# Kernel optimization log

Hardware: AMD Instinct MI355X
Metric: run time of the kernel (lower is better)

The kernel has to match this reference:

```python
import jax, jax.numpy as jnp
import numpy as np

NEG_SLOPE = 0.2


def gat_conv(x, src, dst, W, att_src, att_dst, bias, heads, out_ch, concat):
    """PyG-style GATConv (eval mode, self-loops already appended to src/dst)."""
    N = x.shape[0]
    h = (x @ W).reshape(N, heads, out_ch)                      # [N,H,C]
    a_src = jnp.einsum('nhc,hc->nh', h, att_src)               # [N,H]
    a_dst = jnp.einsum('nhc,hc->nh', h, att_dst)               # [N,H]
    e = jax.nn.leaky_relu(a_src[src] + a_dst[dst], NEG_SLOPE)  # [E,H]
    # numerically-stable softmax segmented by destination node
    emax = jax.ops.segment_max(e, dst, num_segments=N)         # [N,H]
    e = jnp.exp(e - emax[dst])
    denom = jax.ops.segment_sum(e, dst, num_segments=N)
    alpha = e / (denom[dst] + 1e-16)                           # [E,H]
    msg = h[src] * alpha[..., None]                            # [E,H,C]
    out = jax.ops.segment_sum(msg, dst, num_segments=N)        # [N,H,C]
    out = out.reshape(N, heads * out_ch) if concat else out.mean(axis=1)
    return out + bias


def setup_inputs() -> dict:
    key = jax.random.key(0)
    ks = jax.random.split(key, 9)
    N, E, IN, OUT = 100000, 1600000, 128, 40
    H1, C1 = 8, 8
    x = jax.random.normal(ks[0], (N, IN), dtype=jnp.float32)
    edge_index = jax.random.randint(ks[1], (2, E), 0, N, dtype=jnp.int64)
    s = 0.1
    return {
        'x': x,
        'edge_index': edge_index,
        'W1': jax.random.normal(ks[2], (IN, H1 * C1), dtype=jnp.float32) * s,
        'att_src1': jax.random.normal(ks[3], (H1, C1), dtype=jnp.float32) * s,
        'att_dst1': jax.random.normal(ks[4], (H1, C1), dtype=jnp.float32) * s,
        'b1': jnp.zeros((H1 * C1,), dtype=jnp.float32),
        'W2': jax.random.normal(ks[5], (H1 * C1, OUT), dtype=jnp.float32) * s,
        'att_src2': jax.random.normal(ks[6], (1, OUT), dtype=jnp.float32) * s,
        'att_dst2': jax.random.normal(ks[7], (1, OUT), dtype=jnp.float32) * s,
        'b2': jnp.zeros((OUT,), dtype=jnp.float32),
    }


def reference(x, edge_index, W1, att_src1, att_dst1, b1, W2, att_src2, att_dst2, b2):
    N = x.shape[0]
    loops = jnp.arange(N, dtype=edge_index.dtype)
    src = jnp.concatenate([edge_index[0], loops])  # self-loops (PyG default)
    dst = jnp.concatenate([edge_index[1], loops])
    h = gat_conv(x, src, dst, W1, att_src1, att_dst1, b1, 8, 8, True)
    h = jax.nn.elu(h)  # dropout is identity in eval mode
    out = gat_conv(h, src, dst, W2, att_src2, att_dst2, b2, 1, W2.shape[1], False)
    return jax.nn.log_softmax(out, axis=-1)
```

## Files before the change

### kernel.cpp

```cpp
#include <hip/hip_runtime.h>
#include <math.h>

#define NEG_SLOPE 0.2f
#define BSHIFT 8
#define MAXBUK 512

typedef __attribute__((ext_vector_type(8))) short short8;
typedef __attribute__((ext_vector_type(4))) float floatx4;

static __device__ __forceinline__ float lrelu_exp(float e) {
    e = fmaxf(e, NEG_SLOPE * e);
    return __expf(e);
}

static __device__ __forceinline__ short f2bf(float f) {
    union { float f; unsigned u; } v; v.f = f;
    unsigned r = v.u + 0x7FFFu + ((v.u >> 16) & 1u);
    return (short)(r >> 16);
}
static __device__ __forceinline__ float bf2f(unsigned short s) {
    union { float f; unsigned u; } v;
    v.u = ((unsigned)s) << 16;
    return v.f;
}
static __device__ __forceinline__ float bfpair_lo(unsigned v) {
    union { float f; unsigned u; } x; x.u = v << 16; return x.f;
}
static __device__ __forceinline__ float bfpair_hi(unsigned v) {
    union { float f; unsigned u; } x; x.u = v & 0xffff0000u; return x.f;
}
static __device__ __forceinline__ void splitbf(float f, short& hi, short& lo) {
    hi = f2bf(f);
    lo = f2bf(f - bf2f((unsigned short)hi));
}


__global__ __launch_bounds__(512) void k_hist(const int* __restrict__ dst, int E, int CHUNK,
                                              int NBLK, int NBUK, int* __restrict__ blockhist) {
    __shared__ int hist[MAXBUK];
    int t = threadIdx.x, b = blockIdx.x;
    for (int i = t; i < NBUK; i += 512) hist[i] = 0;
    __syncthreads();
    int e0 = b * CHUNK, e1 = e0 + CHUNK; if (e1 > E) e1 = E;
    for (int e = e0 + t; e < e1; e += 512) atomicAdd(&hist[dst[e] >> BSHIFT], 1);
    __syncthreads();
    for (int i = t; i < NBUK; i += 512) blockhist[(size_t)i * NBLK + b] = hist[i];
}

__global__ __launch_bounds__(256) void k_colscan(int* __restrict__ blockhist,
                                                 int* __restrict__ btot, int NBLK) {
    int bucket = blockIdx.x, t = threadIdx.x;
    int lane = t & 63, wv = t >> 6;
    __shared__ int wsum[4];
    __shared__ int carry_s;
    if (t == 0) carry_s = 0;
    __syncthreads();
    for (int base = 0; base < NBLK; base += 256) {
        int idx = base + t;
        int v = (idx < NBLK) ? blockhist[(size_t)bucket * NBLK + idx] : 0;
        int s = v;
#pragma unroll
        for (int o = 1; o < 64; o <<= 1) {
            int u = __shfl_up(s, o, 64);
            if (lane >= o) s += u;
        }
        if (lane == 63) wsum[wv] = s;
        __syncthreads();
        int b0 = 0;
#pragma unroll
        for (int w = 0; w < 4; ++w) b0 += (w < wv) ? wsum[w] : 0;
        int excl = s + b0 - v + carry_s;
        if (idx < NBLK) blockhist[(size_t)bucket * NBLK + idx] = excl;
        __syncthreads();
        if (t == 255) carry_s += s + b0;
        __syncthreads();
    }
    if (t == 0) btot[bucket] = carry_s;
}

__global__ __launch_bounds__(512) void k_bucket_scan(const int* __restrict__ btot,
                                                     int* __restrict__ bucketbase, int NBUK) {
    __shared__ int sh[512];
    int t = threadIdx.x;
    int v = (t < NBUK) ? btot[t] : 0;
    sh[t] = v;
    __syncthreads();
#pragma unroll
    for (int o = 1; o < 512; o <<= 1) {
        int u = (t >= o) ? sh[t - o] : 0;
        __syncthreads();
        sh[t] += u;
        __syncthreads();
    }
    if (t < NBUK) bucketbase[t] = sh[t] - v;
    if (t == NBUK - 1) bucketbase[NBUK] = sh[t];
}

__global__ __launch_bounds__(512) void k_partition(const int* __restrict__ src,
                                                   const int* __restrict__ dst, int E, int CHUNK,
                                                   int NBLK, int NBUK,
                                                   const int* __restrict__ blockhist,
                                                   const int* __restrict__ bucketbase,
                                                   unsigned* __restrict__ packed) {
    __shared__ int cur[MAXBUK];
    int t = threadIdx.x, b = blockIdx.x;
    for (int i = t; i < NBUK; i += 512)
        cur[i] = blockhist[(size_t)i * NBLK + b] + bucketbase[i];
    __syncthreads();
    int e0 = b * CHUNK, e1 = e0 + CHUNK; if (e1 > E) e1 = E;
    for (int e = e0 + t; e < e1; e += 512) {
        int d = dst[e], s = src[e];
        int pos = atomicAdd(&cur[d >> BSHIFT], 1);
        packed[pos] = ((unsigned)s << 8) | ((unsigned)d & 255u);
    }
}

__global__ __launch_bounds__(256) void k_fine(const unsigned* __restrict__ packed,
                                              const int* __restrict__ bucketbase,
                                              int* __restrict__ offsets,
                                              int* __restrict__ csr_src,
                                              int N, int NBUK) {
    __shared__ int fcnt[256];
    __shared__ int wsum[4];
    int bucket = blockIdx.x, t = threadIdx.x;
    int lo = bucket << BSHIFT;
    int nn = N - lo; if (nn > 256) nn = 256;
    int ebase = bucketbase[bucket];
    int ecnt = bucketbase[bucket + 1] - ebase;
    fcnt[t] = 0;
    __syncthreads();
    for (int i = t; i < ecnt; i += 256) {
        unsigned p = packed[ebase + i];
        atomicAdd(&fcnt[p & 255u], 1);
    }
    __syncthreads();
    int v = fcnt[t];
    int lane = t & 63, wv = t >> 6;
    int s = v;
#pragma unroll
    for (int o = 1; o < 64; o <<= 1) {
        int u = __shfl_up(s, o, 64);
        if (lane >= o) s += u;
    }
    if (lane == 63) wsum[wv] = s;
    __syncthreads();
    int base = 0;
#pragma unroll
    for (int w = 0; w < 4; ++w) base += (w < wv) ? wsum[w] : 0;
    int excl = s + base - v;
    if (t < nn) offsets[lo + t] = ebase + excl;
    if (bucket == NBUK - 1 && t == 0) offsets[N] = ebase + ecnt;
    __syncthreads();
    fcnt[t] = excl;
    __syncthreads();
    for (int i = t; i < ecnt; i += 256) {
        unsigned p = packed[ebase + i];
        int pos = atomicAdd(&fcnt[p & 255u], 1);
        csr_src[ebase + pos] = (int)(p >> 8);
    }
}

__global__ __launch_bounds__(256) void k_prepW1(const float* __restrict__ W1,
                                                short* __restrict__ w1t) {
    int i = blockIdx.x * 256 + threadIdx.x;
    if (i < 64 * 128) {
        int n = i >> 7, k = i & 127;
        w1t[i] = f2bf(W1[k * 64 + n]);
    }
}

__global__ __launch_bounds__(256) void k_splitW2(const float* __restrict__ W2,
                                                 short* __restrict__ w2ht,
                                                 short* __restrict__ w2lt) {
    int i = blockIdx.x * 256 + threadIdx.x;
    if (i < 48 * 64) {
        int n = i >> 6, k = i & 63;
        short hi = 0, lo = 0;
        if (n < 40) splitbf(W2[k * 40 + n], hi, lo);
        w2ht[i] = hi; w2lt[i] = lo;
    }
}

__global__ __launch_bounds__(256) void k_gemm1(const float* __restrict__ x,
                                               const short* __restrict__ w1t,
                                               const float* __restrict__ att_s,
                                               const float* __restrict__ att_d,
                                               unsigned short* __restrict__ h1b,
                                               float* __restrict__ a_s1,
                                               float* __restrict__ a_d1, int N) {
    int tid = threadIdx.x, wave = tid >> 6, lane = tid & 63;
    int n16 = lane & 15, q = lane >> 4;
    int nb = blockIdx.x * 64 + wave * 16;
    if (nb >= N) return;

    short8 bfr[4][4];
#pragma unroll
    for (int ct = 0; ct < 4; ++ct) {
        int n = ct * 16 + n16;
#pragma unroll
        for (int kc = 0; kc < 4; ++kc)
            bfr[ct][kc] = *(const short8*)(w1t + n * 128 + kc * 32 + q * 8);
    }

    int arow = nb + n16; if (arow >= N) arow = N - 1;
    const float* xr = x + (size_t)arow * 128 + q * 8;
    short8 afr[4];
#pragma unroll
    for (int kc = 0; kc < 4; ++kc) {
        float4 u0 = *(const float4*)(xr + kc * 32);
        float4 u1 = *(const float4*)(xr + kc * 32 + 4);
        short8 a;
        a[0] = f2bf(u0.x); a[1] = f2bf(u0.y); a[2] = f2bf(u0.z); a[3] = f2bf(u0.w);
        a[4] = f2bf(u1.x); a[5] = f2bf(u1.y); a[6] = f2bf(u1.z); a[7] = f2bf(u1.w);
        afr[kc] = a;
    }

    floatx4 acc[4];
#pragma unroll
    for (int ct = 0; ct < 4; ++ct) {
        floatx4 c = {0.f, 0.f, 0.f, 0.f};
#pragma unroll
        for (int kc = 0; kc < 4; ++kc)
            c = __builtin_amdgcn_mfma_f32_16x16x32_bf16(afr[kc], bfr[ct][kc], c, 0, 0, 0);
        acc[ct] = c;
    }

#pragma unroll
    for (int ct = 0; ct < 4; ++ct) {
#pragma unroll
        for (int r = 0; r < 4; ++r) {
            int row = nb + q * 4 + r;
            if (row < N) h1b[(size_t)row * 64 + ct * 16 + n16] = (unsigned short)f2bf(acc[ct][r]);
        }
    }

#pragma unroll
    for (int ct = 0; ct < 4; ++ct) {
        float as = att_s[ct * 16 + n16];
        float ad = att_d[ct * 16 + n16];
#pragma unroll
        for (int r = 0; r < 4; ++r) {
            float ps = acc[ct][r] * as;
            float pd = acc[ct][r] * ad;
#pragma unroll
            for (int m = 1; m < 8; m <<= 1) {
                ps += __shfl_xor(ps, m, 64);
                pd += __shfl_xor(pd, m, 64);
            }
            int row = nb + q * 4 + r;
            if ((n16 & 7) == 0 && row < N) {
                int h = 2 * ct + (n16 >> 3);
                a_s1[row * 8 + h] = ps;
                a_d1[row * 8 + h] = pd;
            }
        }
    }
}

__global__ __launch_bounds__(256) void k_agg1(const unsigned short* __restrict__ h1b,
                                              const float* __restrict__ a_s1,
                                              const float* __restrict__ a_d1,
                                              const int* __restrict__ offsets,
                                              const int* __restrict__ csr_src,
                                              const float* __restrict__ b1,
                                              float* __restrict__ y1, int N) {
    int wave = threadIdx.x >> 6, lane = threadIdx.x & 63;
    int q = lane >> 4;
    int ll = lane & 15;
    int d = (blockIdx.x * 4 + wave) * 4 + q;
    bool dvalid = (d < N);
    int de = dvalid ? d : N - 1;
    int g = ll >> 3;
    int c = ll & 7;
    float ad = a_d1[de * 8 + c];
    int i0 = offsets[de];
    int deg = dvalid ? (offsets[de + 1] - i0) : 0;
    int dmax = deg;
    dmax = max(dmax, __shfl_xor(dmax, 16, 64));
    dmax = max(dmax, __shfl_xor(dmax, 32, 64));
    float acc[8] = {0.f, 0.f, 0.f, 0.f, 0.f, 0.f, 0.f, 0.f};
    float wsum_l = 0.f;
    if (g == 0) {
        float w0 = lrelu_exp(a_s1[de * 8 + c] + ad);
        uint4 v = *(const uint4*)(h1b + (size_t)de * 64 + 8 * c);
        acc[0] = w0 * bfpair_lo(v.x); acc[1] = w0 * bfpair_hi(v.x);
        acc[2] = w0 * bfpair_lo(v.y); acc[3] = w0 * bfpair_hi(v.y);
        acc[4] = w0 * bfpair_lo(v.z); acc[5] = w0 * bfpair_hi(v.z);
        acc[6] = w0 * bfpair_lo(v.w); acc[7] = w0 * bfpair_hi(v.w);
        wsum_l = w0;
    }
    for (int j = 0; j < dmax; j += 8) {
        int b0 = i0 + j + 4 * g;
        int idx[4]; bool lv[4];
#pragma unroll
        for (int u = 0; u < 4; ++u) {
            int jj = j + 4 * g + u;
            lv[u] = (jj < deg);
            idx[u] = de;
            if (lv[u]) idx[u] = csr_src[b0 + u];
        }
        float ev[4];
#pragma unroll
        for (int u = 0; u < 4; ++u) ev[u] = a_s1[idx[u] * 8 + c] + ad;
        uint4 vv[4];
#pragma unroll
        for (int u = 0; u < 4; ++u)
            vv[u] = *(const uint4*)(h1b + (size_t)idx[u] * 64 + 8 * c);
#pragma unroll
        for (int u = 0; u < 4; ++u) {
            float w = lv[u] ? lrelu_exp(ev[u]) : 0.f;
            wsum_l += w;
            acc[0] = fmaf(w, bfpair_lo(vv[u].x), acc[0]);
            acc[1] = fmaf(w, bfpair_hi(vv[u].x), acc[1]);
            acc[2] = fmaf(w, bfpair_lo(vv[u].y), acc[2]);
            acc[3] = fmaf(w, bfpair_hi(vv[u].y), acc[3]);
            acc[4] = fmaf(w, bfpair_lo(vv[u].z), acc[4]);
            acc[5] = fmaf(w, bfpair_hi(vv[u].z), acc[5]);
            acc[6] = fmaf(w, bfpair_lo(vv[u].w), acc[6]);
            acc[7] = fmaf(w, bfpair_hi(vv[u].w), acc[7]);
        }
    }
#pragma unroll
    for (int k = 0; k < 8; ++k) acc[k] += __shfl(acc[k], lane + 8, 64);
    wsum_l += __shfl(wsum_l, lane + 8, 64);
    if (g == 0 && dvalid) {
        float inv = 1.f / (wsum_l + 1e-16f);
        float4 bA = *(const float4*)(b1 + 8 * c);
        float4 bB = *(const float4*)(b1 + 8 * c + 4);
        float o[8];
        o[0] = acc[0] * inv + bA.x;
        o[1] = acc[1] * inv + bA.y;
        o[2] = acc[2] * inv + bA.z;
        o[3] = acc[3] * inv + bA.w;
        o[4] = acc[4] * inv + bB.x;
        o[5] = acc[5] * inv + bB.y;
        o[6] = acc[6] * inv + bB.z;
        o[7] = acc[7] * inv + bB.w;
#pragma unroll
        for (int k = 0; k < 8; ++k) o[k] = o[k] > 0.f ? o[k] : (__expf(o[k]) - 1.f);
        float4 s0 = make_float4(o[0], o[1], o[2], o[3]);
        float4 s1 = make_float4(o[4], o[5], o[6], o[7]);
        *(float4*)(y1 + (size_t)d * 64 + 8 * c) = s0;
        *(float4*)(y1 + (size_t)d * 64 + 8 * c + 4) = s1;
    }
}

__global__ __launch_bounds__(256) void k_gemm2(const float* __restrict__ y1,
                                               const short* __restrict__ w2ht,
                                               const short* __restrict__ w2lt,
                                               const float* __restrict__ att_s,
                                               const float* __restrict__ att_d,
                                               unsigned short* __restrict__ h2b,
                                               float* __restrict__ a2s,
                                               float* __restrict__ a2d, int N) {
    int tid = threadIdx.x, wave = tid >> 6, lane = tid & 63;
    int n16 = lane & 15, q = lane >> 4;
    int nb = blockIdx.x * 64 + wave * 16;
    if (nb >= N) return;

    int arow = nb + n16; if (arow >= N) arow = N - 1;
    const float* yr = y1 + (size_t)arow * 64 + q * 8;
    short8 ah[2], al[2];
#pragma unroll
    for (int kc = 0; kc < 2; ++kc) {
        float4 u0 = *(const float4*)(yr + kc * 32);
        float4 u1 = *(const float4*)(yr + kc * 32 + 4);
        short8 h, l; short hi, lo;
        splitbf(u0.x, hi, lo); h[0] = hi; l[0] = lo;
        splitbf(u0.y, hi, lo); h[1] = hi; l[1] = lo;
        splitbf(u0.z, hi, lo); h[2] = hi; l[2] = lo;
        splitbf(u0.w, hi, lo); h[3] = hi; l[3] = lo;
        splitbf(u1.x, hi, lo); h[4] = hi; l[4] = lo;
        splitbf(u1.y, hi, lo); h[5] = hi; l[5] = lo;
        splitbf(u1.z, hi, lo); h[6] = hi; l[6] = lo;
        splitbf(u1.w, hi, lo); h[7] = hi; l[7] = lo;
        ah[kc] = h; al[kc] = l;
    }

    float psr[4] = {0.f, 0.f, 0.f, 0.f}, pdr[4] = {0.f, 0.f, 0.f, 0.f};
#pragma unroll
    for (int ct = 0; ct < 3; ++ct) {
        int n = ct * 16 + n16;
        short8 bh0 = *(const short8*)(w2ht + n * 64 + q * 8);
        short8 bh1 = *(const short8*)(w2ht + n * 64 + 32 + q * 8);
        short8 bl0 = *(const short8*)(w2lt + n * 64 + q * 8);
        short8 bl1 = *(const short8*)(w2lt + n * 64 + 32 + q * 8);
        floatx4 c = {0.f, 0.f, 0.f, 0.f};
        c = __builtin_amdgcn_mfma_f32_16x16x32_bf16(ah[0], bl0, c, 0, 0, 0);
        c = __builtin_amdgcn_mfma_f32_16x16x32_bf16(al[0], bh0, c, 0, 0, 0);
        c = __builtin_amdgcn_mfma_f32_16x16x32_bf16(ah[0], bh0, c, 0, 0, 0);
        c = __builtin_amdgcn_mfma_f32_16x16x32_bf16(ah[1], bl1, c, 0, 0, 0);
        c = __builtin_amdgcn_mfma_f32_16x16x32_bf16(al[1], bh1, c, 0, 0, 0);
        c = __builtin_amdgcn_mfma_f32_16x16x32_bf16(ah[1], bh1, c, 0, 0, 0);

        int col = ct * 16 + n16;
#pragma unroll
        for (int r = 0; r < 4; ++r) {
            int row = nb + q * 4 + r;
            if (col < 40 && row < N) h2b[(size_t)row * 40 + col] = (unsigned short)f2bf(c[r]);
        }
        float asv = (col < 40) ? att_s[col] : 0.f;
        float adv = (col < 40) ? att_d[col] : 0.f;
#pragma unroll
        for (int r = 0; r < 4; ++r) {
            psr[r] = fmaf(c[r], asv, psr[r]);
            pdr[r] = fmaf(c[r], adv, pdr[r]);
        }
    }
#pragma unroll
    for (int r = 0; r < 4; ++r) {
        float ps = psr[r], pd = pdr[r];
#pragma unroll
        for (int m = 1; m < 16; m <<= 1) {
            ps += __shfl_xor(ps, m, 64);
            pd += __shfl_xor(pd, m, 64);
        }
        int row = nb + q * 4 + r;
        if (n16 == 0 && row < N) { a2s[row] = ps; a2d[row] = pd; }
    }
}

__global__ __launch_bounds__(256) void k_agg2(const unsigned short* __restrict__ h2b,
                                              const float* __restrict__ a2s,
                                              const float* __restrict__ a2d,
                                              const int* __restrict__ offsets,
                                              const int* __restrict__ csr_src,
                                              const float* __restrict__ b2,
                                              float* __restrict__ out, int N) {
    int wave = threadIdx.x >> 6, lane = threadIdx.x & 63;
    int q = lane >> 4;
    int ll = lane & 15;
    int d = (blockIdx.x * 4 + wave) * 4 + q;
    bool dvalid = (d < N);
    int de = dvalid ? d : N - 1;
    int g = ll / 5;
    int c = ll - g * 5;
    bool lane_ok = (ll < 15);
    float ad = a2d[de];
    float w0 = lrelu_exp(a2s[de] + ad);
    int i0 = offsets[de];
    int deg = offsets[de + 1] - i0;
    if (!dvalid) deg = 0;
    int dmax = deg;
    dmax = max(dmax, __shfl_xor(dmax, 16, 64));
    dmax = max(dmax, __shfl_xor(dmax, 32, 64));
    float acc[8] = {0.f, 0.f, 0.f, 0.f, 0.f, 0.f, 0.f, 0.f};
    float wsum_l = 0.f;
    if (g == 0) {
        uint4 v = *(const uint4*)(h2b + (size_t)de * 40 + 8 * c);
        acc[0] = w0 * bfpair_lo(v.x); acc[1] = w0 * bfpair_hi(v.x);
        acc[2] = w0 * bfpair_lo(v.y); acc[3] = w0 * bfpair_hi(v.y);
        acc[4] = w0 * bfpair_lo(v.z); acc[5] = w0 * bfpair_hi(v.z);
        acc[6] = w0 * bfpair_lo(v.w); acc[7] = w0 * bfpair_hi(v.w);
    }
    for (int j = 0; j < dmax; j += 12) {
        int b0 = i0 + j + 4 * g;
        int idx[4]; bool lv[4];
#pragma unroll
        for (int u = 0; u < 4; ++u) {
            int jj = j + 4 * g + u;
            lv[u] = lane_ok && (jj < deg);
            idx[u] = de;
            if (lv[u]) idx[u] = csr_src[b0 + u];
        }
        float ev[4];
#pragma unroll
        for (int u = 0; u < 4; ++u) ev[u] = a2s[idx[u]] + ad;
        uint4 vv[4];
#pragma unroll
        for (int u = 0; u < 4; ++u)
            vv[u] = *(const uint4*)(h2b + (size_t)idx[u] * 40 + 8 * c);
#pragma unroll
        for (int u = 0; u < 4; ++u) {
            float w = lv[u] ? lrelu_exp(ev[u]) : 0.f;
            if (c == 0) wsum_l += w;
            acc[0] = fmaf(w, bfpair_lo(vv[u].x), acc[0]);
            acc[1] = fmaf(w, bfpair_hi(vv[u].x), acc[1]);
            acc[2] = fmaf(w, bfpair_lo(vv[u].y), acc[2]);
            acc[3] = fmaf(w, bfpair_hi(vv[u].y), acc[3]);
            acc[4] = fmaf(w, bfpair_lo(vv[u].z), acc[4]);
            acc[5] = fmaf(w, bfpair_hi(vv[u].z), acc[5]);
            acc[6] = fmaf(w, bfpair_lo(vv[u].w), acc[6]);
            acc[7] = fmaf(w, bfpair_hi(vv[u].w), acc[7]);
        }
    }
#pragma unroll
    for (int k = 0; k < 8; ++k)
        acc[k] += __shfl(acc[k], lane + 5, 64) + __shfl(acc[k], lane + 10, 64);
    wsum_l += __shfl(wsum_l, lane + 5, 64) + __shfl(wsum_l, lane + 10, 64);
    wsum_l = __shfl(wsum_l, lane & 48, 64);
    float wsum = wsum_l + w0;
    bool act5 = (ll < 5) && dvalid;
    float inv = 1.f / (wsum + 1e-16f);
    float4 bA = *(const float4*)(b2 + 8 * c);
    float4 bB = *(const float4*)(b2 + 8 * c + 4);
    float o[8];
    o[0] = acc[0] * inv + bA.x;
    o[1] = acc[1] * inv + bA.y;
    o[2] = acc[2] * inv + bA.z;
    o[3] = acc[3] * inv + bA.w;
    o[4] = acc[4] * inv + bB.x;
    o[5] = acc[5] * inv + bB.y;
    o[6] = acc[6] * inv + bB.z;
    o[7] = acc[7] * inv + bB.w;
    float mxl = -INFINITY;
    if (act5) {
        mxl = fmaxf(fmaxf(fmaxf(o[0], o[1]), fmaxf(o[2], o[3])),
                    fmaxf(fmaxf(o[4], o[5]), fmaxf(o[6], o[7])));
    }
#pragma unroll
    for (int mm = 1; mm < 8; mm <<= 1) mxl = fmaxf(mxl, __shfl_xor(mxl, mm, 64));
    float exl = 0.f;
    if (act5) {
#pragma unroll
        for (int k = 0; k < 8; ++k) exl += __expf(o[k] - mxl);
    }
#pragma unroll
    for (int mm = 1; mm < 8; mm <<= 1) exl += __shfl_xor(exl, mm, 64);
    if (act5) {
        float lse = mxl + __logf(exl);
        float4 s0 = make_float4(o[0] - lse, o[1] - lse, o[2] - lse, o[3] - lse);
        float4 s1 = make_float4(o[4] - lse, o[5] - lse, o[6] - lse, o[7] - lse);
        *(float4*)(out + (size_t)d * 40 + 8 * c) = s0;
        *(float4*)(out + (size_t)d * 40 + 8 * c + 4) = s1;
    }
}


extern "C" void kernel_launch(void* const* d_in, const int* in_sizes, int n_in,
                              void* d_out, int out_size, void* d_ws, size_t ws_size,
                              hipStream_t stream) {
    const float* x   = (const float*)d_in[0];
    const int*   ei  = (const int*)d_in[1];
    const float* W1  = (const float*)d_in[2];
    const float* as1 = (const float*)d_in[3];
    const float* ad1 = (const float*)d_in[4];
    const float* b1  = (const float*)d_in[5];
    const float* W2  = (const float*)d_in[6];
    const float* as2 = (const float*)d_in[7];
    const float* ad2 = (const float*)d_in[8];
    const float* b2  = (const float*)d_in[9];
    float* out = (float*)d_out;

    int N = in_sizes[0] / 128;
    int E = in_sizes[1] / 2;
    const int* src = ei;
    const int* dst = ei + E;

    int NBUK = (N + 255) >> BSHIFT;
    int CHUNK = 4096;
    int NBLK = (E + CHUNK - 1) / CHUNK;

    char* ws = (char*)d_ws;
    size_t off = 0;
    auto alloc = [&](size_t bytes) -> char* {
        char* p = ws + off;
        off += (bytes + 255) & ~(size_t)255;
        return p;
    };
    unsigned short* h1b = (unsigned short*)alloc((size_t)N * 64 * 2);
    float* a_s1    = (float*)alloc((size_t)N * 8 * 4);
    float* a_d1    = (float*)alloc((size_t)N * 8 * 4);
    float* y1      = (float*)alloc((size_t)N * 64 * 4);
    size_t shared_sz = (size_t)N * 40 * 2;
    if ((size_t)E * 4 > shared_sz) shared_sz = (size_t)E * 4;
    char*  region  = alloc(shared_sz);
    unsigned short* h2b = (unsigned short*)region;
    unsigned* packed    = (unsigned*)region;
    float* a2s     = (float*)alloc((size_t)N * 4);
    float* a2d     = (float*)alloc((size_t)N * 4);
    int*   offsets = (int*)alloc((size_t)(N + 1) * 4);
    int*   csr_src = (int*)alloc((size_t)E * 4);
    int*   blockhist  = (int*)alloc((size_t)NBUK * NBLK * 4);
    int*   btot       = (int*)alloc((size_t)NBUK * 4);
    int*   bucketbase = (int*)alloc((size_t)(NBUK + 1) * 4);
    short* w1t     = (short*)alloc((size_t)64 * 128 * 2);
    short* w2ht    = (short*)alloc((size_t)48 * 64 * 2);
    short* w2lt    = (short*)alloc((size_t)48 * 64 * 2);

    int nb1 = (N + 15) / 16;
    int nb2 = (N + 15) / 16;
    int gb = (N + 63) / 64;

    k_hist<<<NBLK, 512, 0, stream>>>(dst, E, CHUNK, NBLK, NBUK, blockhist);
    k_colscan<<<NBUK, 256, 0, stream>>>(blockhist, btot, NBLK);
    k_bucket_scan<<<1, 512, 0, stream>>>(btot, bucketbase, NBUK);
    k_partition<<<NBLK, 512, 0, stream>>>(src, dst, E, CHUNK, NBLK, NBUK, blockhist,
                                          bucketbase, packed);
    k_fine<<<NBUK, 256, 0, stream>>>(packed, bucketbase, offsets, csr_src, N, NBUK);
    k_prepW1<<<32, 256, 0, stream>>>(W1, w1t);
    k_splitW2<<<12, 256, 0, stream>>>(W2, w2ht, w2lt);
    k_gemm1<<<gb, 256, 0, stream>>>(x, w1t, as1, ad1, h1b, a_s1, a_d1, N);
    k_agg1<<<nb1, 256, 0, stream>>>(h1b, a_s1, a_d1, offsets, csr_src, b1, y1, N);
    k_gemm2<<<gb, 256, 0, stream>>>(y1, w2ht, w2lt, as2, ad2, h2b, a2s, a2d, N);
    k_agg2<<<nb2, 256, 0, stream>>>(h2b, a2s, a2d, offsets, csr_src, b2, out, N);
}
```

Baseline: 180.0 us.

## Fuse weight prep into histogram and gemm1 into partition launches

Weight conversion blocks are appended to the histogram kernel, and the first-layer GEMM blocks are appended to the partition kernel, so the two independent streams of work share launches and overlap. This removes three kernel launches and lets the dense GEMM fill the GPU while the scatter-heavy partition runs. The h2b row stride is also padded from 40 to 48 elements for aligned gathers, at the cost of extra memory and bandwidth. The gemm1 part now uses 512-thread blocks covering 128 rows.

```diff
diff --git a/kernel.cpp b/kernel.cpp
--- a/kernel.cpp
+++ b/kernel.cpp
@@ -35,16 +35,36 @@
 }
 
 
-__global__ __launch_bounds__(512) void k_hist(const int* __restrict__ dst, int E, int CHUNK,
-                                              int NBLK, int NBUK, int* __restrict__ blockhist) {
+__global__ __launch_bounds__(512) void k_hist_prep(const int* __restrict__ dst, int E, int CHUNK,
+                                                   int NBLK, int NBUK,
+                                                   int* __restrict__ blockhist,
+                                                   const float* __restrict__ W1,
+                                                   short* __restrict__ w1t,
+                                                   const float* __restrict__ W2,
+                                                   short* __restrict__ w2ht,
+                                                   short* __restrict__ w2lt) {
     __shared__ int hist[MAXBUK];
     int t = threadIdx.x, b = blockIdx.x;
-    for (int i = t; i < NBUK; i += 512) hist[i] = 0;
-    __syncthreads();
-    int e0 = b * CHUNK, e1 = e0 + CHUNK; if (e1 > E) e1 = E;
-    for (int e = e0 + t; e < e1; e += 512) atomicAdd(&hist[dst[e] >> BSHIFT], 1);
-    __syncthreads();
-    for (int i = t; i < NBUK; i += 512) blockhist[(size_t)i * NBLK + b] = hist[i];
+    if (b < NBLK) {
+        for (int i = t; i < NBUK; i += 512) hist[i] = 0;
+        __syncthreads();
+        int e0 = b * CHUNK, e1 = e0 + CHUNK; if (e1 > E) e1 = E;
+        for (int e = e0 + t; e < e1; e += 512) atomicAdd(&hist[dst[e] >> BSHIFT], 1);
+        __syncthreads();
+        for (int i = t; i < NBUK; i += 512) blockhist[(size_t)i * NBLK + b] = hist[i];
+    } else {
+        int i = (b - NBLK) * 512 + t;
+        if (i < 64 * 128) {
+            int n = i >> 7, k = i & 127;
+            w1t[i] = f2bf(W1[k * 64 + n]);
+        } else if (i < 64 * 128 + 48 * 64) {
+            int j = i - 64 * 128;
+            int n = j >> 6, k = j & 63;
+            short hi = 0, lo = 0;
+            if (n < 40) splitbf(W2[k * 40 + n], hi, lo);
+            w2ht[j] = hi; w2lt[j] = lo;
+        }
+    }
 }
 
 __global__ __launch_bounds__(256) void k_colscan(int* __restrict__ blockhist,
@@ -96,22 +116,99 @@
     if (t == NBUK - 1) bucketbase[NBUK] = sh[t];
 }
 
-__global__ __launch_bounds__(512) void k_partition(const int* __restrict__ src,
-                                                   const int* __restrict__ dst, int E, int CHUNK,
-                                                   int NBLK, int NBUK,
-                                                   const int* __restrict__ blockhist,
-                                                   const int* __restrict__ bucketbase,
-                                                   unsigned* __restrict__ packed) {
+__global__ __launch_bounds__(512) void k_part_gemm1(const int* __restrict__ src,
+                                                    const int* __restrict__ dst, int E, int CHUNK,
+                                                    int NBLK, int NBUK,
+                                                    const int* __restrict__ blockhist,
+                                                    const int* __restrict__ bucketbase,
+                                                    unsigned* __restrict__ packed,
+                                                    const float* __restrict__ x,
+                                                    const short* __restrict__ w1t,
+                                                    const float* __restrict__ att_s,
+                                                    const float* __restrict__ att_d,
+                                                    unsigned short* __restrict__ h1b,
+                                                    float* __restrict__ a_s1,
+                                                    float* __restrict__ a_d1, int N) {
     __shared__ int cur[MAXBUK];
     int t = threadIdx.x, b = blockIdx.x;
-    for (int i = t; i < NBUK; i += 512)
-        cur[i] = blockhist[(size_t)i * NBLK + b] + bucketbase[i];
-    __syncthreads();
-    int e0 = b * CHUNK, e1 = e0 + CHUNK; if (e1 > E) e1 = E;
-    for (int e = e0 + t; e < e1; e += 512) {
-        int d = dst[e], s = src[e];
-        int pos = atomicAdd(&cur[d >> BSHIFT], 1);
-        packed[pos] = ((unsigned)s << 8) | ((unsigned)d & 255u);
+    if (b < NBLK) {
+        for (int i = t; i < NBUK; i += 512)
+            cur[i] = blockhist[(size_t)i * NBLK + b] + bucketbase[i];
+        __syncthreads();
+        int e0 = b * CHUNK, e1 = e0 + CHUNK; if (e1 > E) e1 = E;
+        for (int e = e0 + t; e < e1; e += 512) {
+            int d = dst[e], s = src[e];
+            int pos = atomicAdd(&cur[d >> BSHIFT], 1);
+            packed[pos] = ((unsigned)s << 8) | ((unsigned)d & 255u);
+        }
+        return;
+    }
+    int wave = t >> 6, lane = t & 63;
+    int n16 = lane & 15, q = lane >> 4;
+    int nb = (b - NBLK) * 128 + wave * 16;
+    if (nb >= N) return;
+
+    short8 bfr[4][4];
+#pragma unroll
+    for (int ct = 0; ct < 4; ++ct) {
+        int n = ct * 16 + n16;
+#pragma unroll
+        for (int kc = 0; kc < 4; ++kc)
+            bfr[ct][kc] = *(const short8*)(w1t + n * 128 + kc * 32 + q * 8);
+    }
+
+    int arow = nb + n16; if (arow >= N) arow = N - 1;
+    const float* xr = x + (size_t)arow * 128 + q * 8;
+    short8 afr[4];
+#pragma unroll
+    for (int kc = 0; kc < 4; ++kc) {
+        float4 u0 = *(const float4*)(xr + kc * 32);
+        float4 u1 = *(const float4*)(xr + kc * 32 + 4);
+        short8 a;
+        a[0] = f2bf(u0.x); a[1] = f2bf(u0.y); a[2] = f2bf(u0.z); a[3] = f2bf(u0.w);
+        a[4] = f2bf(u1.x); a[5] = f2bf(u1.y); a[6] = f2bf(u1.z); a[7] = f2bf(u1.w);
+        afr[kc] = a;
+    }
+
+    floatx4 acc[4];
+#pragma unroll
+    for (int ct = 0; ct < 4; ++ct) {
+        floatx4 c = {0.f, 0.f, 0.f, 0.f};
+#pragma unroll
+        for (int kc = 0; kc < 4; ++kc)
+            c = __builtin_amdgcn_mfma_f32_16x16x32_bf16(afr[kc], bfr[ct][kc], c, 0, 0, 0);
+        acc[ct] = c;
+    }
+
+#pragma unroll
+    for (int ct = 0; ct < 4; ++ct) {
+#pragma unroll
+        for (int r = 0; r < 4; ++r) {
+            int row = nb + q * 4 + r;
+            if (row < N) h1b[(size_t)row * 64 + ct * 16 + n16] = (unsigned short)f2bf(acc[ct][r]);
+        }
+    }
+
+#pragma unroll
+    for (int ct = 0; ct < 4; ++ct) {
+        float as = att_s[ct * 16 + n16];
+        float ad = att_d[ct * 16 + n16];
+#pragma unroll
+        for (int r = 0; r < 4; ++r) {
+            float ps = acc[ct][r] * as;
+            float pd = acc[ct][r] * ad;
+#pragma unroll
+            for (int m = 1; m < 8; m <<= 1) {
+                ps += __shfl_xor(ps, m, 64);
+                pd += __shfl_xor(pd, m, 64);
+            }
+            int row = nb + q * 4 + r;
+            if ((n16 & 7) == 0 && row < N) {
+                int h = 2 * ct + (n16 >> 3);
+                a_s1[row * 8 + h] = ps;
+                a_d1[row * 8 + h] = pd;
+            }
+        }
     }
 }
 
@@ -157,103 +254,6 @@
         unsigned p = packed[ebase + i];
         int pos = atomicAdd(&fcnt[p & 255u], 1);
         csr_src[ebase + pos] = (int)(p >> 8);
-    }
-}
-
-__global__ __launch_bounds__(256) void k_prepW1(const float* __restrict__ W1,
-                                                short* __restrict__ w1t) {
-    int i = blockIdx.x * 256 + threadIdx.x;
-    if (i < 64 * 128) {
-        int n = i >> 7, k = i & 127;
-        w1t[i] = f2bf(W1[k * 64 + n]);
-    }
-}
-
-__global__ __launch_bounds__(256) void k_splitW2(const float* __restrict__ W2,
-                                                 short* __restrict__ w2ht,
-                                                 short* __restrict__ w2lt) {
-    int i = blockIdx.x * 256 + threadIdx.x;
-    if (i < 48 * 64) {
-        int n = i >> 6, k = i & 63;
-        short hi = 0, lo = 0;
-        if (n < 40) splitbf(W2[k * 40 + n], hi, lo);
-        w2ht[i] = hi; w2lt[i] = lo;
-    }
-}
-
-__global__ __launch_bounds__(256) void k_gemm1(const float* __restrict__ x,
-                                               const short* __restrict__ w1t,
-                                               const float* __restrict__ att_s,
-                                               const float* __restrict__ att_d,
-                                               unsigned short* __restrict__ h1b,
-                                               float* __restrict__ a_s1,
-                                               float* __restrict__ a_d1, int N) {
-    int tid = threadIdx.x, wave = tid >> 6, lane = tid & 63;
-    int n16 = lane & 15, q = lane >> 4;
-    int nb = blockIdx.x * 64 + wave * 16;
-    if (nb >= N) return;
-
-    short8 bfr[4][4];
-#pragma unroll
-    for (int ct = 0; ct < 4; ++ct) {
-        int n = ct * 16 + n16;
-#pragma unroll
-        for (int kc = 0; kc < 4; ++kc)
-            bfr[ct][kc] = *(const short8*)(w1t + n * 128 + kc * 32 + q * 8);
-    }
-
-    int arow = nb + n16; if (arow >= N) arow = N - 1;
-    const float* xr = x + (size_t)arow * 128 + q * 8;
-    short8 afr[4];
-#pragma unroll
-    for (int kc = 0; kc < 4; ++kc) {
-        float4 u0 = *(const float4*)(xr + kc * 32);
-        float4 u1 = *(const float4*)(xr + kc * 32 + 4);
-        short8 a;
-        a[0] = f2bf(u0.x); a[1] = f2bf(u0.y); a[2] = f2bf(u0.z); a[3] = f2bf(u0.w);
-        a[4] = f2bf(u1.x); a[5] = f2bf(u1.y); a[6] = f2bf(u1.z); a[7] = f2bf(u1.w);
-        afr[kc] = a;
-    }
-
-    floatx4 acc[4];
-#pragma unroll
-    for (int ct = 0; ct < 4; ++ct) {
-        floatx4 c = {0.f, 0.f, 0.f, 0.f};
-#pragma unroll
-        for (int kc = 0; kc < 4; ++kc)
-            c = __builtin_amdgcn_mfma_f32_16x16x32_bf16(afr[kc], bfr[ct][kc], c, 0, 0, 0);
-        acc[ct] = c;
-    }
-
-#pragma unroll
-    for (int ct = 0; ct < 4; ++ct) {
-#pragma unroll
-        for (int r = 0; r < 4; ++r) {
-            int row = nb + q * 4 + r;
-            if (row < N) h1b[(size_t)row * 64 + ct * 16 + n16] = (unsigned short)f2bf(acc[ct][r]);
-        }
-    }
-
-#pragma unroll
-    for (int ct = 0; ct < 4; ++ct) {
-        float as = att_s[ct * 16 + n16];
-        float ad = att_d[ct * 16 + n16];
-#pragma unroll
-        for (int r = 0; r < 4; ++r) {
-            float ps = acc[ct][r] * as;
-            float pd = acc[ct][r] * ad;
-#pragma unroll
-            for (int m = 1; m < 8; m <<= 1) {
-                ps += __shfl_xor(ps, m, 64);
-                pd += __shfl_xor(pd, m, 64);
-            }
-            int row = nb + q * 4 + r;
-            if ((n16 & 7) == 0 && row < N) {
-                int h = 2 * ct + (n16 >> 3);
-                a_s1[row * 8 + h] = ps;
-                a_d1[row * 8 + h] = pd;
-            }
-        }
     }
 }
 
@@ -397,7 +397,7 @@
 #pragma unroll
         for (int r = 0; r < 4; ++r) {
             int row = nb + q * 4 + r;
-            if (col < 40 && row < N) h2b[(size_t)row * 40 + col] = (unsigned short)f2bf(c[r]);
+            if (col < 40 && row < N) h2b[(size_t)row * 48 + col] = (unsigned short)f2bf(c[r]);
         }
         float asv = (col < 40) ? att_s[col] : 0.f;
         float adv = (col < 40) ? att_d[col] : 0.f;
@@ -447,7 +447,7 @@
     float acc[8] = {0.f, 0.f, 0.f, 0.f, 0.f, 0.f, 0.f, 0.f};
     float wsum_l = 0.f;
     if (g == 0) {
-        uint4 v = *(const uint4*)(h2b + (size_t)de * 40 + 8 * c);
+        uint4 v = *(const uint4*)(h2b + (size_t)de * 48 + 8 * c);
         acc[0] = w0 * bfpair_lo(v.x); acc[1] = w0 * bfpair_hi(v.x);
         acc[2] = w0 * bfpair_lo(v.y); acc[3] = w0 * bfpair_hi(v.y);
         acc[4] = w0 * bfpair_lo(v.z); acc[5] = w0 * bfpair_hi(v.z);
@@ -469,7 +469,7 @@
         uint4 vv[4];
 #pragma unroll
         for (int u = 0; u < 4; ++u)
-            vv[u] = *(const uint4*)(h2b + (size_t)idx[u] * 40 + 8 * c);
+            vv[u] = *(const uint4*)(h2b + (size_t)idx[u] * 48 + 8 * c);
 #pragma unroll
         for (int u = 0; u < 4; ++u) {
             float w = lv[u] ? lrelu_exp(ev[u]) : 0.f;
@@ -562,7 +562,7 @@
     float* a_s1    = (float*)alloc((size_t)N * 8 * 4);
     float* a_d1    = (float*)alloc((size_t)N * 8 * 4);
     float* y1      = (float*)alloc((size_t)N * 64 * 4);
-    size_t shared_sz = (size_t)N * 40 * 2;
+    size_t shared_sz = (size_t)N * 48 * 2;
     if ((size_t)E * 4 > shared_sz) shared_sz = (size_t)E * 4;
     char*  region  = alloc(shared_sz);
     unsigned short* h2b = (unsigned short*)region;
@@ -580,18 +580,19 @@
 
     int nb1 = (N + 15) / 16;
     int nb2 = (N + 15) / 16;
-    int gb = (N + 63) / 64;
-
-    k_hist<<<NBLK, 512, 0, stream>>>(dst, E, CHUNK, NBLK, NBUK, blockhist);
+    int gb2 = (N + 63) / 64;
+    int GB1 = (N + 127) / 128;
+    int PREPB = 22;
+
+    k_hist_prep<<<NBLK + PREPB, 512, 0, stream>>>(dst, E, CHUNK, NBLK, NBUK, blockhist,
+                                                  W1, w1t, W2, w2ht, w2lt);
     k_colscan<<<NBUK, 256, 0, stream>>>(blockhist, btot, NBLK);
     k_bucket_scan<<<1, 512, 0, stream>>>(btot, bucketbase, NBUK);
-    k_partition<<<NBLK, 512, 0, stream>>>(src, dst, E, CHUNK, NBLK, NBUK, blockhist,
-                                          bucketbase, packed);
+    k_part_gemm1<<<NBLK + GB1, 512, 0, stream>>>(src, dst, E, CHUNK, NBLK, NBUK, blockhist,
+                                                 bucketbase, packed,
+                                                 x, w1t, as1, ad1, h1b, a_s1, a_d1, N);
     k_fine<<<NBUK, 256, 0, stream>>>(packed, bucketbase, offsets, csr_src, N, NBUK);
-    k_prepW1<<<32, 256, 0, stream>>>(W1, w1t);
-    k_splitW2<<<12, 256, 0, stream>>>(W2, w2ht, w2lt);
-    k_gemm1<<<gb, 256, 0, stream>>>(x, w1t, as1, ad1, h1b, a_s1, a_d1, N);
     k_agg1<<<nb1, 256, 0, stream>>>(h1b, a_s1, a_d1, offsets, csr_src, b1, y1, N);
-    k_gemm2<<<gb, 256, 0, stream>>>(y1, w2ht, w2lt, as2, ad2, h2b, a2s, a2d, N);
+    k_gemm2<<<gb2, 256, 0, stream>>>(y1, w2ht, w2lt, as2, ad2, h2b, a2s, a2d, N);
     k_agg2<<<nb2, 256, 0, stream>>>(h2b, a2s, a2d, offsets, csr_src, b2, out, N);
 }
```

Result: faster. 171.4 us (-4.8%).
